# Kernel optimization log

Hardware: AMD Instinct MI355X
Metric: run time of the kernel (lower is better)

## Reference

```python
import jax, jax.numpy as jnp
import numpy as np

K = 2
ALPHA = 1.0
EPS = 1e-6


def _bce_logits(x, z):
    # binary_cross_entropy_with_logits, elementwise, numerically stable
    return jax.nn.softplus(x) - x * z


def _unfold(x, i):
    # F.unfold(x, kernel_size=2i+1, padding=i) for x: [B,1,H,W] -> [B, P, H*W]
    ks = 2 * i + 1
    p = jax.lax.conv_general_dilated_patches(
        x, (ks, ks), (1, 1), [(i, i), (i, i)])  # [B, ks*ks, H, W], zero-padded
    B = x.shape[0]
    return p.reshape(B, ks * ks, -1)


def setup_inputs() -> dict:
    key = jax.random.key(0)
    k1, k2 = jax.random.split(key)
    B, H, W = 8, 512, 512
    pred = jax.random.normal(k1, (B, 1, H, W), dtype=jnp.float32)
    target = jax.random.randint(k2, (B, 1, H, W), 0, 2).astype(jnp.float32)
    return {"pred": pred, "target": target}


def reference(pred, target):
    B, _, H, W = pred.shape
    N = H * W
    bce = _bce_logits(pred, target).reshape(B, 1, N)  # [B,1,N]
    total = jnp.zeros((B, N), dtype=pred.dtype)
    for i in range(1, K + 1):
        ks = 2 * i + 1
        P = ks * ks
        c = P // 2
        up = _unfold(pred, i)                      # [B,P,N]
        ut = _unfold(target, i)                    # [B,P,N]
        vm = _unfold(jnp.ones_like(target), i) == 0  # True where padding
        cp = up[:, c:c + 1, :]                     # center logits [B,1,N]
        ct = ut[:, c:c + 1, :]
        joint = cp * up
        lab = ct * ut
        mutual = _bce_logits(joint, lab)
        pairwise = jnp.exp(-jax.nn.sigmoid(cp) * jax.nn.sigmoid(up))
        loss = bce / (mutual + ALPHA * pairwise + EPS)
        loss = jnp.where(vm, jnp.asarray(1.0, loss.dtype), loss)
        total = total + (0.5 ** (i - 1)) * (loss.sum(axis=1) / P)
    return total.mean()
```

## Files before the change

kernel.cpp:

```cpp
#include <hip/hip_runtime.h>

#define TILE 32
#define HALO 2
#define LH (TILE + HALO)
#define LW (TILE + 2 * HALO)
#define HT 512
#define WD 512

typedef _Float16 h2 __attribute__((ext_vector_type(2)));

constexpr float W_IN  = 1.0f / 9.0f + 0.02f;
constexpr float W_OUT = 0.02f;
constexpr float INV_D_OOB = 0.590364f;


__device__ __forceinline__ h2 pk2(float a, float b) {
    return __builtin_bit_cast(h2, __builtin_amdgcn_cvt_pkrtz(a, b));
}
__device__ __forceinline__ h2 hsp(float x) {
    h2 r; r.x = (_Float16)x; r.y = (_Float16)x; return r;
}
__device__ __forceinline__ h2 mkh(float a, float b) {
    h2 r; r.x = (_Float16)a; r.y = (_Float16)b; return r;
}

struct FracH { h2 n, d; };

__device__ __forceinline__ FracH pair2h(float cax, h2 cay, h2 caz, h2 caw,
                                        const float4 cb1, const float4 cb2, h2 wv) {
    const float j1 = cax * cb1.x, j2 = cax * cb2.x;
    const h2 J = pk2(j1, j2);
    const h2 U = pk2(__expf(-fabsf(j1)), __expf(-fabsf(j2)));
    const h2 T = pk2(cb1.y, cb2.y);
    const h2 G = pk2(cb1.z, cb2.z);
    const h2 Wb = pk2(cb1.w, cb2.w);
    h2 L = __builtin_elementwise_fma(U, hsp(0.098765f), hsp(-0.370370f));
    L = __builtin_elementwise_fma(L, U, hsp(0.962963f));
    L = __builtin_elementwise_fma(L, U, hsp(0.004231f));
    const h2 LAB = T * cay;
    const h2 mx = __builtin_elementwise_max(J, hsp(0.f));
    h2 m = __builtin_elementwise_fma(-J, LAB, mx);
    m = m + L;
    const h2 GG = G * caz;
    h2 E = __builtin_elementwise_fma(GG, hsp(-0.101088f), hsp(0.454898f));
    E = __builtin_elementwise_fma(E, GG, hsp(-0.985612f));
    E = __builtin_elementwise_fma(E, GG, hsp(0.998280f));
    FracH r;
    r.d = m + E;
    r.n = (Wb + caw) * wv;
    return r;
}

__device__ __forceinline__ FracH mergeh(FracH a, FracH b) {
    FracH r;
    r.n = __builtin_elementwise_fma(a.n, b.d, a.d * b.n);
    r.d = a.d * b.d;
    return r;
}

__global__ __launch_bounds__(256) void scloss_main(
    const float* __restrict__ pred, const float* __restrict__ target,
    float* __restrict__ out, double inv_cnt) {
    __shared__ float4 sh[LH * LW];

    const int b = blockIdx.x >> 8;
    const int tile = blockIdx.x & 255;
    const int ty0 = (tile >> 4) << 5;
    const int tx0 = (tile & 15) << 5;

    const float* pbase = pred + ((size_t)b << 18);
    const float* tbase = target + ((size_t)b << 18);
    const int tid = threadIdx.x;

    int cy = tid / LW;
    int cx = tid - cy * LW;
    #pragma unroll
    for (int i = 0; i < 5; ++i) {
        const int idx = tid + (i << 8);
        if (idx < LH * LW) {
            const int gy = ty0 + cy;
            const int gx = tx0 + cx - HALO;
            float p = 0.f, t = 0.f, g = 0.f, bce = 0.f;
            if ((unsigned)gx < (unsigned)WD && gy < HT) {
                const int gi = (gy << 9) + gx;
                p = pbase[gi];
                t = tbase[gi];
                const float en = __expf(-fabsf(p));
                const float inv = __builtin_amdgcn_rcpf(1.f + en);
                g = (p >= 0.f) ? inv : en * inv;
                float L = fmaf(fmaf(fmaf(0.098765f, en, -0.370370f), en,
                                    0.962963f), en, 0.004231f);
                bce = fmaf(-p, t, fmaxf(p, 0.f)) + L;
            }
            sh[idx] = make_float4(p, t, g, bce);
        }
        cx += 4; cy += 7;
        if (cx >= LW) { cx -= LW; ++cy; }
    }
    __syncthreads();

    const int px = tid & 31;
    const int py0 = tid >> 5;
    float acc = 0.f;

    const bool edge = (tx0 == 0) | (tx0 == WD - TILE) | (ty0 == 0) | (ty0 == HT - TILE);

    constexpr int pdy[12] = {0, 0, 1, 1, 1, 1, 1, 2, 2, 2, 2, 2};
    constexpr int pdx[12] = {1, 2, -2, -1, 0, 1, 2, -2, -1, 0, 1, 2};
    constexpr float pw12[12] = {W_IN, W_OUT, W_OUT, W_IN, W_IN, W_IN,
                                W_OUT, W_OUT, W_OUT, W_OUT, W_OUT, W_OUT};

    #pragma unroll
    for (int r = 0; r < 4; ++r) {
        const int ay = py0 + (r << 3);
        const float4* base = &sh[ay * LW + px + HALO];
        const float4 ca = base[0];

        const h2 cay = hsp(ca.y), caz = pk2(ca.z, ca.z), caw = pk2(ca.w, ca.w);

        const float j0 = ca.x * ca.x;
        const float u0 = __expf(-j0);
        const float L0 = fmaf(fmaf(fmaf(0.098765f, u0, -0.370370f), u0,
                                   0.962963f), u0, 0.004231f);
        const float m0 = fmaf(-j0, ca.y * ca.y, j0) + L0;
        const float gg0 = ca.z * ca.z;
        const float E0 = fmaf(fmaf(fmaf(-0.101088f, gg0, 0.454898f), gg0,
                                   -0.985612f), gg0, 0.998280f);
        const float d0 = m0 + E0;
        const float n0 = W_IN * ca.w;

        const FracH F1 = pair2h(ca.x, cay, caz, caw, base[1],          base[2],          mkh(W_IN,  W_OUT));
        const FracH F2 = pair2h(ca.x, cay, caz, caw, base[LW - 2],     base[LW - 1],     mkh(W_OUT, W_IN));
        const FracH F3 = pair2h(ca.x, cay, caz, caw, base[LW],         base[LW + 1],     mkh(W_IN,  W_IN));
        const FracH F4 = pair2h(ca.x, cay, caz, caw, base[LW + 2],     base[2 * LW - 2], mkh(W_OUT, W_OUT));
        const FracH F5 = pair2h(ca.x, cay, caz, caw, base[2 * LW - 1], base[2 * LW],     mkh(W_OUT, W_OUT));
        const FracH F6 = pair2h(ca.x, cay, caz, caw, base[2 * LW + 1], base[2 * LW + 2], mkh(W_OUT, W_OUT));

        const FracH A = mergeh(F1, F2);
        const FracH Bb = mergeh(F3, F4);
        const FracH C = mergeh(F5, F6);
        const FracH D2 = mergeh(A, Bb);
        const FracH G2 = mergeh(D2, C);

        const float nl = (float)G2.n.x, nh = (float)G2.n.y;
        const float dl = (float)G2.d.x, dh = (float)G2.d.y;
        const float Nt = fmaf(nl, dh, nh * dl), Dt = dl * dh;
        const float Nf = fmaf(n0, Dt, Nt * d0), Df = d0 * Dt;
        acc = fmaf(Nf, __builtin_amdgcn_rcpf(Df), acc);

        if (edge) {
            const int gy = ty0 + ay, gx = tx0 + px;
            #pragma unroll
            for (int k = 0; k < 12; ++k) {
                if (gy + pdy[k] >= HT || gx + pdx[k] < 0 || gx + pdx[k] >= WD)
                    acc += pw12[k] * (1.f - ca.w * INV_D_OOB);
                if (gy - pdy[k] < 0 || gx - pdx[k] < 0 || gx - pdx[k] >= WD)
                    acc += pw12[k];
            }
        }
    }

    #pragma unroll
    for (int off = 32; off > 0; off >>= 1)
        acc += __shfl_down(acc, off, 64);
    __shared__ double wsum[4];
    if ((tid & 63) == 0) wsum[tid >> 6] = (double)acc;
    __syncthreads();
    if (tid == 0) {
        const double s = wsum[0] + wsum[1] + wsum[2] + wsum[3];
        atomicAdd(out, (float)(s * inv_cnt));
    }
}

extern "C" void kernel_launch(void* const* d_in, const int* in_sizes, int n_in,
                              void* d_out, int out_size, void* d_ws, size_t ws_size,
                              hipStream_t stream) {
    const float* pred   = (const float*)d_in[0];
    const float* target = (const float*)d_in[1];
    float* out = (float*)d_out;

    const int B = in_sizes[0] / (HT * WD);
    const int nblocks = B * 256;

    (void)hipMemsetAsync(out, 0, sizeof(float), stream);
    scloss_main<<<nblocks, 256, 0, stream>>>(pred, target, out,
                                             1.0 / ((double)B * HT * WD));
}
```

Measured before the change: 97.55 us.

## Shrink tiles to 16x16 and replace atomic accumulation with two-pass reduction

Tiles shrink from 32x32 to 16x16, so each thread computes one output pixel instead of four and the grid has four times as many blocks. The float atomicAdd into the output is replaced by per-block double partials written to the workspace, followed by a single-block reduction kernel, which also removes the memset. Smaller tiles raise the halo overhead (the shared tile grows from 34x36 to 18x20, about 1.4 loaded elements per output instead of about 1.2) and repeat the BCE/sigmoid preprocessing on the halo, and the extra kernel launch adds a serial tail, in exchange for more parallelism and no atomic contention.

Measured after the change: 92.04 us. 5.7% less time.

```diff
diff --git a/kernel.cpp b/kernel.cpp
--- a/kernel.cpp
+++ b/kernel.cpp
@@ -1,6 +1,6 @@
 #include <hip/hip_runtime.h>
 
-#define TILE 32
+#define TILE 16
 #define HALO 2
 #define LH (TILE + HALO)
 #define LW (TILE + 2 * HALO)
@@ -60,24 +60,24 @@
 
 __global__ __launch_bounds__(256) void scloss_main(
     const float* __restrict__ pred, const float* __restrict__ target,
-    float* __restrict__ out, double inv_cnt) {
+    double* __restrict__ partial) {
     __shared__ float4 sh[LH * LW];
 
-    const int b = blockIdx.x >> 8;
-    const int tile = blockIdx.x & 255;
-    const int ty0 = (tile >> 4) << 5;
-    const int tx0 = (tile & 15) << 5;
+    const int b = blockIdx.x >> 10;
+    const int tile = blockIdx.x & 1023;
+    const int ty0 = (tile >> 5) << 4;
+    const int tx0 = (tile & 31) << 4;
 
     const float* pbase = pred + ((size_t)b << 18);
     const float* tbase = target + ((size_t)b << 18);
     const int tid = threadIdx.x;
 
-    int cy = tid / LW;
-    int cx = tid - cy * LW;
     #pragma unroll
-    for (int i = 0; i < 5; ++i) {
+    for (int i = 0; i < 2; ++i) {
         const int idx = tid + (i << 8);
         if (idx < LH * LW) {
+            const int cy = idx / LW;
+            const int cx = idx - cy * LW;
             const int gy = ty0 + cy;
             const int gx = tx0 + cx - HALO;
             float p = 0.f, t = 0.f, g = 0.f, bce = 0.f;
@@ -94,13 +94,11 @@
             }
             sh[idx] = make_float4(p, t, g, bce);
         }
-        cx += 4; cy += 7;
-        if (cx >= LW) { cx -= LW; ++cy; }
     }
     __syncthreads();
 
-    const int px = tid & 31;
-    const int py0 = tid >> 5;
+    const int px = tid & 15;
+    const int py = tid >> 4;
     float acc = 0.f;
 
     const bool edge = (tx0 == 0) | (tx0 == WD - TILE) | (ty0 == 0) | (ty0 == HT - TILE);
@@ -110,10 +108,8 @@
     constexpr float pw12[12] = {W_IN, W_OUT, W_OUT, W_IN, W_IN, W_IN,
                                 W_OUT, W_OUT, W_OUT, W_OUT, W_OUT, W_OUT};
 
-    #pragma unroll
-    for (int r = 0; r < 4; ++r) {
-        const int ay = py0 + (r << 3);
-        const float4* base = &sh[ay * LW + px + HALO];
+    {
+        const float4* base = &sh[py * LW + px + HALO];
         const float4 ca = base[0];
 
         const h2 cay = hsp(ca.y), caz = pk2(ca.z, ca.z), caw = pk2(ca.w, ca.w);
@@ -149,7 +145,7 @@
         acc = fmaf(Nf, __builtin_amdgcn_rcpf(Df), acc);
 
         if (edge) {
-            const int gy = ty0 + ay, gx = tx0 + px;
+            const int gy = ty0 + py, gx = tx0 + px;
             #pragma unroll
             for (int k = 0; k < 12; ++k) {
                 if (gy + pdy[k] >= HT || gx + pdx[k] < 0 || gx + pdx[k] >= WD)
@@ -166,10 +162,23 @@
     __shared__ double wsum[4];
     if ((tid & 63) == 0) wsum[tid >> 6] = (double)acc;
     __syncthreads();
-    if (tid == 0) {
-        const double s = wsum[0] + wsum[1] + wsum[2] + wsum[3];
-        atomicAdd(out, (float)(s * inv_cnt));
+    if (tid == 0)
+        partial[blockIdx.x] = wsum[0] + wsum[1] + wsum[2] + wsum[3];
+}
+
+__global__ __launch_bounds__(256) void scloss_reduce(
+    const double* __restrict__ partial, int n, float* __restrict__ out,
+    double inv_cnt) {
+    __shared__ double sm[256];
+    double s = 0.0;
+    for (int i = threadIdx.x; i < n; i += 256) s += partial[i];
+    sm[threadIdx.x] = s;
+    __syncthreads();
+    for (int off = 128; off > 0; off >>= 1) {
+        if (threadIdx.x < off) sm[threadIdx.x] += sm[threadIdx.x + off];
+        __syncthreads();
     }
+    if (threadIdx.x == 0) out[0] = (float)(sm[0] * inv_cnt);
 }
 
 extern "C" void kernel_launch(void* const* d_in, const int* in_sizes, int n_in,
@@ -180,9 +189,10 @@
     float* out = (float*)d_out;
 
     const int B = in_sizes[0] / (HT * WD);
-    const int nblocks = B * 256;
+    const int nblocks = B * 1024;
 
-    (void)hipMemsetAsync(out, 0, sizeof(float), stream);
-    scloss_main<<<nblocks, 256, 0, stream>>>(pred, target, out,
-                                             1.0 / ((double)B * HT * WD));
+    double* partial = (double*)d_ws;
+    scloss_main<<<nblocks, 256, 0, stream>>>(pred, target, partial);
+    scloss_reduce<<<1, 256, 0, stream>>>(partial, nblocks, out,
+                                         1.0 / ((double)B * HT * WD));
 }
```
